# Optimization experiments

Measured on AMD Instinct MI355X. Metric: run time of the kernel, lower is better.

The kernel has to match this reference:

```python
import jax, jax.numpy as jnp
import numpy as np
from functools import partial

B, EMB, H, V, T = 128, 512, 1024, 8192, 100
START_VALUE = 0


def setup_inputs() -> dict:
    key = jax.random.key(0)
    ks = jax.random.split(key, 8)
    s = 0.05
    return {
        "x": jax.random.normal(ks[0], (B, H), jnp.float32),
        "emb_table": jax.random.normal(ks[1], (V, EMB), jnp.float32) * s,
        "w_ih": jax.random.normal(ks[2], (3 * H, EMB), jnp.float32) * s,
        "w_hh": jax.random.normal(ks[3], (3 * H, H), jnp.float32) * s,
        "b_ih": jax.random.normal(ks[4], (3 * H,), jnp.float32) * s,
        "b_hh": jax.random.normal(ks[5], (3 * H,), jnp.float32) * s,
        "cls_w": jax.random.normal(ks[6], (V, H), jnp.float32) * s,
        "cls_b": jax.random.normal(ks[7], (V,), jnp.float32) * s,
    }


def _gru_cell(e, h, w_ih, w_hh, b_ih, b_hh):
    # PyTorch GRU cell math. e: [B,EMB], h: [B,H]
    gi = e @ w_ih.T + b_ih  # [B, 3H]
    gh = h @ w_hh.T + b_hh  # [B, 3H]
    i_r, i_z, i_n = jnp.split(gi, 3, axis=1)
    h_r, h_z, h_n = jnp.split(gh, 3, axis=1)
    r = jax.nn.sigmoid(i_r + h_r)
    z = jax.nn.sigmoid(i_z + h_z)
    n = jnp.tanh(i_n + r * h_n)
    return (1.0 - z) * n + z * h


def reference(x, emb_table, w_ih, w_hh, b_ih, b_hh, cls_w, cls_b):
    # start distribution: log_softmax of one-hot at START_VALUE
    start_val = jax.nn.log_softmax(
        jnp.zeros((V,), x.dtype).at[START_VALUE].set(1.0), axis=0
    )
    prev0 = jnp.broadcast_to(start_val, (B, V))

    def step(carry, _):
        h, prev_logp = carry
        idx = jnp.argmax(prev_logp, axis=1)          # [B]
        e = emb_table[idx]                           # [B, EMB]
        h_new = _gru_cell(e, h, w_ih, w_hh, b_ih, b_hh)
        logp = jax.nn.log_softmax(h_new @ cls_w.T + cls_b, axis=1)  # [B, V]
        return (h_new, logp), logp

    _, outs = jax.lax.scan(step, (x, prev0), None, length=T - 1)
    outs = jnp.transpose(outs, (1, 0, 2))            # [B, T-1, V]
    return jnp.concatenate([prev0[:, None, :], outs], axis=1)  # [B, T, V]
```

## Files before the change

kernel.cpp:

```cpp
#include <hip/hip_runtime.h>
#include <stdint.h>


#define Bb   128
#define EMBd 512
#define Hd   1024
#define Vd   8192
#define Td   100
#define HPB  524288

typedef __attribute__((ext_vector_type(8))) _Float16 half8;
typedef __attribute__((ext_vector_type(4))) float f32x4;
typedef unsigned long long ull;

#define LOSCALE 2048.0f
#define LOINV   (1.0f/2048.0f)

#define WAITV(N) do { asm volatile("s_waitcnt vmcnt(" #N ")" ::: "memory"); \
                      __builtin_amdgcn_sched_barrier(0); } while (0)

__device__ __forceinline__ uint32_t fkey(float f) {
  uint32_t u = __float_as_uint(f);
  return (u & 0x80000000u) ? ~u : (u | 0x80000000u);
}
__device__ __forceinline__ ull umax64(ull a, ull b) { return a > b ? a : b; }

__device__ __forceinline__ void dma16(const void* g, void* l) {
  __builtin_amdgcn_global_load_lds((const uint32_t*)g, (uint32_t*)l, 16, 0, 0);
}
__device__ __forceinline__ void st16sc(void* p, half8 v) {
  f32x4 d = *(f32x4*)&v;
  asm volatile("global_store_dwordx4 %0, %1, off sc0 sc1"
               :: "v"(p), "v"(d) : "memory");
}
__device__ __forceinline__ ull sysld64(const ull* p) {
  return __hip_atomic_load((ull*)p, __ATOMIC_RELAXED, __HIP_MEMORY_SCOPE_SYSTEM);
}
__device__ __forceinline__ uint32_t ld32sys(uint32_t* p) {
  return __hip_atomic_load(p, __ATOMIC_RELAXED, __HIP_MEMORY_SCOPE_SYSTEM);
}
__device__ __forceinline__ void st32sys(uint32_t* p, uint32_t v) {
  __hip_atomic_store(p, v, __ATOMIC_RELAXED, __HIP_MEMORY_SCOPE_SYSTEM);
}
__device__ __forceinline__ uint32_t add32sys(uint32_t* p, uint32_t v) {
  return __hip_atomic_fetch_add(p, v, __ATOMIC_RELAXED, __HIP_MEMORY_SCOPE_SYSTEM);
}

__device__ __forceinline__ void cvt8(const float4 v0, const float4 v1,
                                     half8& hh, half8& ll) {
  float vv[8] = {v0.x, v0.y, v0.z, v0.w, v1.x, v1.y, v1.z, v1.w};
#pragma unroll
  for (int i = 0; i < 8; ++i) {
    _Float16 h = (_Float16)vv[i];
    hh[i] = h;
    ll[i] = (_Float16)((vv[i] - (float)h) * LOSCALE);
  }
}

__global__ void k_init(const float* __restrict__ x, float* __restrict__ hbuf0,
                       ull* __restrict__ amax, char* __restrict__ hpre0,
                       uint32_t* __restrict__ bar) {
  int tid = blockIdx.x * 256 + threadIdx.x;
  if (tid < Bb * Hd) hbuf0[tid] = x[tid];
  if (tid < Td * Bb) amax[tid] = (tid < Bb) ? 0xFFFFFFFFull : 0ull;
  if (tid >= 16384 && tid < 16640)
    bar[tid - 16384] = (tid - 16384 == 8) ? 128u : 0u;
  if (tid < 16384) {
    int b = tid & 127, sc = tid >> 7;
    int st = sc >> 2, c = sc & 3;
    const float* src = x + b * Hd + st * 32 + c * 8;
    float4 v0 = *(const float4*)src, v1 = *(const float4*)(src + 4);
    half8 hh, ll; cvt8(v0, v1, hh, ll);
    char* hp = hpre0 + st * 16384 + b * 128;
    *(half8*)(hp + ((c       ^ (b & 7))) * 16) = hh;
    *(half8*)(hp + (((c + 4) ^ (b & 7))) * 16) = ll;
  }
}

__global__ void k_prep_emb(const float* __restrict__ emb, char* __restrict__ embp) {
  int t = blockIdx.x * 256 + threadIdx.x;
  int row = t >> 6, rem = t & 63, st = rem >> 2, c = rem & 3;
  const float* src = emb + (size_t)row * EMBd + st * 32 + c * 8;
  float4 v0 = *(const float4*)src, v1 = *(const float4*)(src + 4);
  half8 hh, ll; cvt8(v0, v1, hh, ll);
  char* d = embp + (size_t)row * 2048 + st * 128;
  *(half8*)(d + c * 16) = hh;
  *(half8*)(d + (c + 4) * 16) = ll;
}

__global__ void k_prep_w(const float* __restrict__ w_ih, const float* __restrict__ w_hh,
                         char* __restrict__ wpre) {
  int bi = blockIdx.x;
  int st = bi % 12, t2 = bi / 12, q = t2 & 3, cg = t2 >> 2;
  int t = threadIdx.x; if (t >= 192) return;
  int r = t >> 2, c = t & 3;
  int g = r >> 4, bn = r & 15;
  int k0 = q * 384 + st * 32 + c * 8;
  const float* src = (k0 < 512)
    ? (w_ih + (size_t)(g * 1024 + cg * 16 + bn) * EMBd + k0)
    : (w_hh + (size_t)(g * 1024 + cg * 16 + bn) * Hd + (k0 - 512));
  float4 v0 = *(const float4*)src, v1 = *(const float4*)(src + 4);
  half8 hh, ll; cvt8(v0, v1, hh, ll);
  char* d = wpre + (size_t)bi * 6144 + r * 128;
  *(half8*)(d + ((c       ^ (r & 7))) * 16) = hh;
  *(half8*)(d + (((c + 4) ^ (r & 7))) * 16) = ll;
}

__global__ void k_prep_cls(const float* __restrict__ cls_w, char* __restrict__ clsp) {
  int b = blockIdx.x;
  int ct = b >> 5, st = b & 31;
  int t = threadIdx.x;
  int r = t >> 2, c = t & 3;
  const float* src = cls_w + (size_t)(ct * 64 + r) * Hd + st * 32 + c * 8;
  float4 v0 = *(const float4*)src, v1 = *(const float4*)(src + 4);
  half8 hh, ll; cvt8(v0, v1, hh, ll);
  char* d = clsp + (size_t)b * 8192 + r * 128;
  *(half8*)(d + ((c       ^ (r & 7))) * 16) = hh;
  *(half8*)(d + (((c + 4) ^ (r & 7))) * 16) = ll;
}

__global__ __launch_bounds__(256, 2) void k_prep_gi(
    const char* __restrict__ embp, const char* __restrict__ wpre,
    const float* __restrict__ b_ih, float* __restrict__ gi)
{
  const int cg = blockIdx.x, vh = blockIdx.y;
  const int tid = threadIdx.x, lane = tid & 63, w = tid >> 6;
  const int C = cg * 16;
  __shared__ __align__(16) char pA[4 * 8192];
  __shared__ __align__(16) char pB[4 * 6144];

  f32x4 accH[3], accL[3];
#pragma unroll
  for (int g = 0; g < 3; ++g) {
    accH[g] = (f32x4){0.f, 0.f, 0.f, 0.f};
    accL[g] = (f32x4){0.f, 0.f, 0.f, 0.f};
  }

  const int rr = lane >> 3, cc = lane & 7;
  const char* abase = embp + (size_t)(vh * 64 + w * 16 + rr) * 2048 + ((cc ^ rr) * 16);

  auto issue = [&](int st) {
    char* da = pA + (st & 3) * 8192 + w * 2048;
    const char* s0 = abase + st * 128;
    dma16(s0, da);
    dma16(s0 + 8 * 2048, da + 1024);
    const int wq = st / 12, wst = st - wq * 12;
    const char* sb = wpre + (size_t)((cg * 4 + wq) * 12 + wst) * 6144 + w * 1536 + lane * 16;
    char* db = pB + (st & 3) * 6144 + w * 1536;
    dma16(sb, db);
    if (lane < 32) dma16(sb + 1024, db + 1024);
  };

  const int l15 = lane & 15, qd = lane >> 4, r7 = l15 & 7;
  const int offAH = (w * 16 + l15) * 128 + ((qd)     ^ r7) * 16;
  const int offAL = (w * 16 + l15) * 128 + ((qd + 4) ^ r7) * 16;

  issue(0); issue(1); issue(2);
  WAITV(8);
  __builtin_amdgcn_s_barrier();

  for (int st = 0; st < 16; ++st) {
    const int bf = st & 3;
    half8 aH = *(half8*)&pA[bf * 8192 + offAH];
    half8 aL = *(half8*)&pA[bf * 8192 + offAL];
    if (st + 3 < 16) issue(st + 3);
#pragma unroll
    for (int g = 0; g < 3; ++g) {
      half8 bH = *(half8*)&pB[bf * 6144 + (g * 16 + l15) * 128 + ((qd)     ^ r7) * 16];
      half8 bL = *(half8*)&pB[bf * 6144 + (g * 16 + l15) * 128 + ((qd + 4) ^ r7) * 16];
      accH[g] = __builtin_amdgcn_mfma_f32_16x16x32_f16(aH, bH, accH[g], 0, 0, 0);
      accL[g] = __builtin_amdgcn_mfma_f32_16x16x32_f16(aH, bL, accL[g], 0, 0, 0);
      accL[g] = __builtin_amdgcn_mfma_f32_16x16x32_f16(aL, bH, accL[g], 0, 0, 0);
    }
    if (st < 15) {
      if (st <= 12)      { WAITV(8); }
      else if (st == 13) { WAITV(4); }
      else               { WAITV(0); }
      asm volatile("s_waitcnt lgkmcnt(0)" ::: "memory");
      __builtin_amdgcn_sched_barrier(0);
      __builtin_amdgcn_s_barrier();
    }
  }

  const int v0 = vh * 64 + w * 16 + qd * 4;
#pragma unroll
  for (int g = 0; g < 3; ++g) {
    float bi = b_ih[g * 1024 + C + l15];
#pragma unroll
    for (int i = 0; i < 4; ++i) {
      float val = accH[g][i] + accL[g][i] * LOINV + bi;
      gi[(size_t)(v0 + i) * 3072 + g * 1024 + C + l15] = val;
    }
  }
}

__global__ __launch_bounds__(256) void k_loop(
    const char* __restrict__ wpre, const char* __restrict__ clsp,
    const float* __restrict__ gi,
    const float* __restrict__ b_hh, const float* __restrict__ cls_b,
    float* __restrict__ hbuf, char* __restrict__ hpre,
    ull* __restrict__ amax, float* __restrict__ out,
    uint32_t* __restrict__ bar)
{
  const int wg = blockIdx.x;
  const int tid = threadIdx.x, lane = tid & 63, w = tid >> 6;
  __shared__ __align__(16) char smem[149504];

  if (tid == 0)
    (void)__hip_atomic_load(&bar[200], __ATOMIC_ACQUIRE, __HIP_MEMORY_SCOPE_AGENT);
  __syncthreads();

  uint32_t* gCnt   = &bar[0];
  uint32_t* hReady = &bar[1];
  uint32_t* aCnt   = &bar[8];

  const int l15 = lane & 15, qd = lane >> 4, r7 = l15 & 7;
  const int offA_H = (w * 16 + l15) * 128 + ((qd)     ^ r7) * 16;
  const int offA_L = (w * 16 + l15) * 128 + ((qd + 4) ^ r7) * 16;

  if (wg < 128) {
    const int cg = wg & 63, rh = wg >> 6;
    const int C = cg * 16;
    char* gA = smem;
    char* gB = smem + 49152;

    for (int s = 1; s < Td; ++s) {
      if (tid == 0)
        while (ld32sys(hReady) < (uint32_t)(s - 1)) __builtin_amdgcn_s_sleep(2);
      __syncthreads();

      const char* hsrc = hpre + (size_t)(s - 1) * HPB + rh * 8192 + w * 2048 + lane * 16;

      f32x4 accH[3], accL[3];
#pragma unroll
      for (int g = 0; g < 3; ++g) {
        accH[g] = (f32x4){0.f, 0.f, 0.f, 0.f};
        accL[g] = (f32x4){0.f, 0.f, 0.f, 0.f};
      }

      auto issue = [&](int st) {
        const int bf = st % 6;
        char* da = gA + bf * 8192 + w * 2048;
        const char* sa = hsrc + st * 16384;
        dma16(sa, da);
        dma16(sa + 1024, da + 1024);
        const int k0 = 512 + st * 32;
        const int wq = (k0 >= 1152) ? 3 : (k0 >= 768 ? 2 : 1);
        const int wst = (k0 - wq * 384) >> 5;
        const char* sb = wpre + (size_t)((cg * 4 + wq) * 12 + wst) * 6144 + w * 1536 + lane * 16;
        char* db = gB + bf * 6144 + w * 1536;
        dma16(sb, db);
        if (lane < 32) dma16(sb + 1024, db + 1024);
      };

      issue(0); issue(1); issue(2); issue(3); issue(4);

      for (int st = 0; st < 32; ++st) {
        if (st <= 27)      { WAITV(12); }
        else if (st == 28) { WAITV(9); }
        else if (st == 29) { WAITV(6); }
        else if (st == 30) { WAITV(3); }
        else               { WAITV(0); }
        __builtin_amdgcn_s_barrier();

        const int bf = st % 6;
        half8 aH = *(half8*)&gA[bf * 8192 + offA_H];
        half8 aL = *(half8*)&gA[bf * 8192 + offA_L];
        if (st + 5 < 32) issue(st + 5);
#pragma unroll
        for (int g = 0; g < 3; ++g) {
          half8 bH = *(half8*)&gB[bf * 6144 + (g * 16 + l15) * 128 + ((qd)     ^ r7) * 16];
          half8 bL = *(half8*)&gB[bf * 6144 + (g * 16 + l15) * 128 + ((qd + 4) ^ r7) * 16];
          accH[g] = __builtin_amdgcn_mfma_f32_16x16x32_f16(aH, bH, accH[g], 0, 0, 0);
          accL[g] = __builtin_amdgcn_mfma_f32_16x16x32_f16(aH, bL, accL[g], 0, 0, 0);
          accL[g] = __builtin_amdgcn_mfma_f32_16x16x32_f16(aL, bH, accL[g], 0, 0, 0);
        }
      }

      if (tid == 0)
        while (ld32sys(&aCnt[s - 1]) < 128u) __builtin_amdgcn_s_sleep(2);
      __syncthreads();

      const int j = C + l15;
      const float bh0 = b_hh[j], bh1 = b_hh[1024 + j], bh2 = b_hh[2048 + j];
      const float* hprev_f = hbuf + (size_t)((s - 1) & 1) * Bb * Hd;
      float* hnew_f = hbuf + (size_t)(s & 1) * Bb * Hd;
      const ull* amax_prev = amax + (size_t)(s - 1) * Bb;
      float outs[4];
#pragma unroll
      for (int i = 0; i < 4; ++i) {
        const int ri = rh * 64 + w * 16 + qd * 4 + i;
        const uint32_t idx = (~(uint32_t)sysld64(&amax_prev[ri])) & 8191u;
        const float* gp = gi + (size_t)idx * 3072 + j;
        float i_r = gp[0], i_z = gp[1024], i_n = gp[2048];
        float h_r = accH[0][i] + accL[0][i] * LOINV + bh0;
        float h_z = accH[1][i] + accL[1][i] * LOINV + bh1;
        float h_n = accH[2][i] + accL[2][i] * LOINV + bh2;
        float rr2 = 1.f / (1.f + expf(-(i_r + h_r)));
        float zz = 1.f / (1.f + expf(-(i_z + h_z)));
        float nn = tanhf(i_n + rr2 * h_n);
        float o = (1.f - zz) * nn + zz * hprev_f[ri * Hd + j];
        hnew_f[ri * Hd + j] = o;
        outs[i] = o;
      }
      __syncthreads();
      float* sT = (float*)smem;
#pragma unroll
      for (int i = 0; i < 4; ++i)
        sT[(w * 16 + qd * 4 + i) * 16 + l15] = outs[i];
      __syncthreads();
      if (tid < 128) {
        const int row = tid >> 1, half = tid & 1;
        const int b = rh * 64 + row;
        const float* srcp = sT + row * 16 + half * 8;
        half8 hh, ll;
#pragma unroll
        for (int e = 0; e < 8; ++e) {
          float o = srcp[e];
          _Float16 oh = (_Float16)o;
          hh[e] = oh;
          ll[e] = (_Float16)((o - (float)oh) * LOSCALE);
        }
        const int stp = C >> 5;
        const int chb = ((C & 31) >> 3) + half;
        char* hp = hpre + (size_t)s * HPB + stp * 16384 + b * 128;
        st16sc(hp + ((chb       ^ (b & 7))) * 16, hh);
        st16sc(hp + (((chb + 4) ^ (b & 7))) * 16, ll);
      }
      WAITV(0);
      __syncthreads();
      if (tid == 0) {
        uint32_t old = add32sys(gCnt, 1u);
        if (old + 1u == 128u * (uint32_t)s)
          st32sys(hReady, (uint32_t)s);
      }
    }
  } else {
    const int wgC = wg - 128;
    const int ct2 = wgC & 63, rt0 = wgC >> 6;
    const int r0c = rt0 * 64;
    char* cA = smem;
    char* cB = smem + 49152;
    const char* bb0 = clsp + (size_t)(2 * ct2)     * 262144 + w * 2048 + lane * 16;
    const char* bb1 = clsp + (size_t)(2 * ct2 + 1) * 262144 + w * 2048 + lane * 16;

    for (int s = 1; s < Td; ++s) {
      if (tid == 0)
        while (ld32sys(hReady) < (uint32_t)s) __builtin_amdgcn_s_sleep(2);
      __syncthreads();

      const char* asrc = hpre + (size_t)s * HPB + rt0 * 8192 + w * 2048 + lane * 16;

      f32x4 accH[8], accL[8];
#pragma unroll
      for (int i = 0; i < 8; ++i) {
        accH[i] = (f32x4){0.f, 0.f, 0.f, 0.f};
        accL[i] = (f32x4){0.f, 0.f, 0.f, 0.f};
      }

      auto issue = [&](int st) {
        const int bf = st % 6;
        char* da = cA + bf * 8192 + w * 2048;
        const char* sa = asrc + st * 16384;
        dma16(sa, da);
        dma16(sa + 1024, da + 1024);
        char* db = cB + bf * 16384 + w * 2048;
        const char* s0 = bb0 + st * 8192;
        dma16(s0, db);
        dma16(s0 + 1024, db + 1024);
        const char* s1 = bb1 + st * 8192;
        dma16(s1, db + 8192);
        dma16(s1 + 1024, db + 8192 + 1024);
      };

      issue(0); issue(1); issue(2); issue(3); issue(4);

      for (int st = 0; st < 32; ++st) {
        if (st <= 27)      { WAITV(24); }
        else if (st == 28) { WAITV(18); }
        else if (st == 29) { WAITV(12); }
        else if (st == 30) { WAITV(6); }
        else               { WAITV(0); }
        __builtin_amdgcn_s_barrier();

        const int bf = st % 6;
        half8 aH = *(half8*)&cA[bf * 8192 + offA_H];
        half8 aL = *(half8*)&cA[bf * 8192 + offA_L];
        if (st + 5 < 32) issue(st + 5);
#pragma unroll
        for (int cf = 0; cf < 8; ++cf) {
          const int bo = bf * 16384 + (cf >> 2) * 8192 + ((cf & 3) * 16 + l15) * 128;
          half8 bH = *(half8*)&cB[bo + ((qd)     ^ r7) * 16];
          half8 bL = *(half8*)&cB[bo + ((qd + 4) ^ r7) * 16];
          accH[cf] = __builtin_amdgcn_mfma_f32_16x16x32_f16(aH, bH, accH[cf], 0, 0, 0);
          accL[cf] = __builtin_amdgcn_mfma_f32_16x16x32_f16(aH, bL, accL[cf], 0, 0, 0);
          accL[cf] = __builtin_amdgcn_mfma_f32_16x16x32_f16(aL, bH, accL[cf], 0, 0, 0);
        }
      }

      float bsv[8];
#pragma unroll
      for (int cf = 0; cf < 8; ++cf)
        bsv[cf] = cls_b[(2 * ct2 + (cf >> 2)) * 64 + (cf & 3) * 16 + l15];
#pragma unroll
      for (int i = 0; i < 4; ++i) {
        const int brow = r0c + w * 16 + qd * 4 + i;
        float* orow = out + ((size_t)brow * Td + s) * Vd;
        ull best = 0ull;
#pragma unroll
        for (int cf = 0; cf < 8; ++cf) {
          const int v = (2 * ct2 + (cf >> 2)) * 64 + (cf & 3) * 16 + l15;
          float val = accH[cf][i] + accL[cf][i] * LOINV + bsv[cf];
          __builtin_nontemporal_store(val, &orow[v]);
          best = umax64(best, ((ull)fkey(val) << 32) | (uint32_t)(~(uint32_t)v));
        }
        best = umax64(best, __shfl_xor(best, 1));
        best = umax64(best, __shfl_xor(best, 2));
        best = umax64(best, __shfl_xor(best, 4));
        best = umax64(best, __shfl_xor(best, 8));
        if (l15 == 0) atomicMax(&amax[(size_t)s * Bb + brow], best);
      }
      WAITV(0);
      __syncthreads();
      if (tid == 0) add32sys(&aCnt[s], 1u);
    }
  }
}

__global__ void k_softmax(float* __restrict__ out,
                          const ull* __restrict__ amax) {
  int blk = blockIdx.x;
  int t = blk % Td, b = blk / Td;
  int tid = threadIdx.x;
  float* row = out + ((size_t)b * Td + t) * Vd;
  if (t == 0) {
    float lse0 = logf(expf(1.0f) + (float)(Vd - 1));
    for (int i = tid; i < Vd; i += 256) row[i] = ((i == 0) ? 1.0f : 0.0f) - lse0;
    return;
  }
  ull key = amax[t * Bb + b];
  uint32_t ku = (uint32_t)(key >> 32);
  uint32_t u = (ku & 0x80000000u) ? (ku & 0x7fffffffu) : ~ku;
  float m = __uint_as_float(u);
  float x[32];
  float ssum = 0.f;
#pragma unroll
  for (int i = 0; i < 32; ++i) {
    x[i] = row[tid + i * 256];
    ssum += expf(x[i] - m);
  }
  ssum += __shfl_xor(ssum, 1);
  ssum += __shfl_xor(ssum, 2);
  ssum += __shfl_xor(ssum, 4);
  ssum += __shfl_xor(ssum, 8);
  ssum += __shfl_xor(ssum, 16);
  ssum += __shfl_xor(ssum, 32);
  __shared__ float wsum[4];
  if ((tid & 63) == 0) wsum[tid >> 6] = ssum;
  __syncthreads();
  float lse = m + logf(wsum[0] + wsum[1] + wsum[2] + wsum[3]);
#pragma unroll
  for (int i = 0; i < 32; ++i) row[tid + i * 256] = x[i] - lse;
}

extern "C" void kernel_launch(void* const* d_in, const int* in_sizes, int n_in,
                              void* d_out, int out_size, void* d_ws, size_t ws_size,
                              hipStream_t stream) {
  const float* x     = (const float*)d_in[0];
  const float* emb   = (const float*)d_in[1];
  const float* w_ih  = (const float*)d_in[2];
  const float* w_hh  = (const float*)d_in[3];
  const float* b_ih  = (const float*)d_in[4];
  const float* b_hh  = (const float*)d_in[5];
  const float* cls_w = (const float*)d_in[6];
  const float* cls_b = (const float*)d_in[7];
  float* out = (float*)d_out;

  char* ws = (char*)d_ws;
  size_t o = 0;
  ull*      amax = (ull*)(ws + o);      o += (size_t)Td * Bb * 8;
  uint32_t* bar  = (uint32_t*)(ws + o); o += 1024;
  float*    hbuf = (float*)(ws + o);    o += (size_t)2 * Bb * Hd * 4;
  char*     hpre = ws + o;              o += (size_t)Td * HPB;
  char*     embp = ws + o;              o += (size_t)Vd * 2048;
  char*     wpre = ws + o;              o += (size_t)3072 * 6144;
  char*     clsp = ws + o;              o += (size_t)128 * 32 * 8192;
  float*    gi   = (float*)(ws + o);    o += (size_t)Vd * 3072 * 4;

  k_init<<<512, 256, 0, stream>>>(x, hbuf, amax, hpre, bar);
  k_prep_emb<<<2048, 256, 0, stream>>>(emb, embp);
  k_prep_w<<<3072, 256, 0, stream>>>(w_ih, w_hh, wpre);
  k_prep_cls<<<4096, 256, 0, stream>>>(cls_w, clsp);
  k_prep_gi<<<dim3(64, 128), 256, 0, stream>>>(embp, wpre, b_ih, gi);

  k_loop<<<256, 256, 0, stream>>>(wpre, clsp, gi, b_hh, cls_b,
                                  hbuf, hpre, amax, out, bar);

  k_softmax<<<12800, 256, 0, stream>>>(out, amax);
}
```

Before: 4.524 ms.

## Use hierarchical padded barrier counters and pad argmax slots to avoid atomic contention

Replaces the single global arrival counters for the GRU and classifier groups with a two-level tree. Groups of 8 workgroups first increment their own counter, each padded to 128 bytes, and the last arrival bumps a top-level counter. The per-row argmax atomicMax slots are also spaced 128 bytes apart so that concurrent atomics from different rows do not share a cache line. The aim is to cut serialization of contended atomics on the per-step critical path, at the cost of an extra atomic hop for the last arrival and a larger workspace.

Measured after the change: 3.849 ms. 1.18x faster.

```diff
diff --git a/kernel.cpp b/kernel.cpp
--- a/kernel.cpp
+++ b/kernel.cpp
@@ -8,6 +8,7 @@
 #define Vd   8192
 #define Td   100
 #define HPB  524288
+#define AST  16
 
 typedef __attribute__((ext_vector_type(8))) _Float16 half8;
 typedef __attribute__((ext_vector_type(4))) float f32x4;
@@ -15,6 +16,8 @@
 
 #define LOSCALE 2048.0f
 #define LOINV   (1.0f/2048.0f)
+
+#define BAR_WORDS 65536
 
 #define WAITV(N) do { asm volatile("s_waitcnt vmcnt(" #N ")" ::: "memory"); \
                       __builtin_amdgcn_sched_barrier(0); } while (0)
@@ -62,9 +65,10 @@
                        uint32_t* __restrict__ bar) {
   int tid = blockIdx.x * 256 + threadIdx.x;
   if (tid < Bb * Hd) hbuf0[tid] = x[tid];
-  if (tid < Td * Bb) amax[tid] = (tid < Bb) ? 0xFFFFFFFFull : 0ull;
-  if (tid >= 16384 && tid < 16640)
-    bar[tid - 16384] = (tid - 16384 == 8) ? 128u : 0u;
+  if (tid < Td * Bb)
+    amax[(size_t)tid * AST] = (tid < Bb) ? 0xFFFFFFFFull : 0ull;
+  if (tid < BAR_WORDS)
+    bar[tid] = (tid == 1024) ? 16u : 0u;
   if (tid < 16384) {
     int b = tid & 127, sc = tid >> 7;
     int st = sc >> 2, c = sc & 3;
@@ -207,12 +211,10 @@
   __shared__ __align__(16) char smem[149504];
 
   if (tid == 0)
-    (void)__hip_atomic_load(&bar[200], __ATOMIC_ACQUIRE, __HIP_MEMORY_SCOPE_AGENT);
+    (void)__hip_atomic_load(&bar[576], __ATOMIC_ACQUIRE, __HIP_MEMORY_SCOPE_AGENT);
   __syncthreads();
 
-  uint32_t* gCnt   = &bar[0];
-  uint32_t* hReady = &bar[1];
-  uint32_t* aCnt   = &bar[8];
+  uint32_t* hReady = &bar[544];
 
   const int l15 = lane & 15, qd = lane >> 4, r7 = l15 & 7;
   const int offA_H = (w * 16 + l15) * 128 + ((qd)     ^ r7) * 16;
@@ -278,19 +280,19 @@
       }
 
       if (tid == 0)
-        while (ld32sys(&aCnt[s - 1]) < 128u) __builtin_amdgcn_s_sleep(2);
+        while (ld32sys(&bar[1024 + (s - 1) * 32]) < 16u) __builtin_amdgcn_s_sleep(2);
       __syncthreads();
 
       const int j = C + l15;
       const float bh0 = b_hh[j], bh1 = b_hh[1024 + j], bh2 = b_hh[2048 + j];
       const float* hprev_f = hbuf + (size_t)((s - 1) & 1) * Bb * Hd;
       float* hnew_f = hbuf + (size_t)(s & 1) * Bb * Hd;
-      const ull* amax_prev = amax + (size_t)(s - 1) * Bb;
+      const ull* amax_prev = amax + (size_t)(s - 1) * Bb * AST;
       float outs[4];
 #pragma unroll
       for (int i = 0; i < 4; ++i) {
         const int ri = rh * 64 + w * 16 + qd * 4 + i;
-        const uint32_t idx = (~(uint32_t)sysld64(&amax_prev[ri])) & 8191u;
+        const uint32_t idx = (~(uint32_t)sysld64(&amax_prev[(size_t)ri * AST])) & 8191u;
         const float* gp = gi + (size_t)idx * 3072 + j;
         float i_r = gp[0], i_z = gp[1024], i_n = gp[2048];
         float h_r = accH[0][i] + accL[0][i] * LOINV + bh0;
@@ -330,9 +332,12 @@
       WAITV(0);
       __syncthreads();
       if (tid == 0) {
-        uint32_t old = add32sys(gCnt, 1u);
-        if (old + 1u == 128u * (uint32_t)s)
-          st32sys(hReady, (uint32_t)s);
+        uint32_t old = add32sys(&bar[(wg >> 3) * 32], 1u);
+        if (old + 1u == 8u * (uint32_t)s) {
+          uint32_t o2 = add32sys(&bar[512], 1u);
+          if (o2 + 1u == 16u * (uint32_t)s)
+            st32sys(hReady, (uint32_t)s);
+        }
       }
     }
   } else {
@@ -418,11 +423,16 @@
         best = umax64(best, __shfl_xor(best, 2));
         best = umax64(best, __shfl_xor(best, 4));
         best = umax64(best, __shfl_xor(best, 8));
-        if (l15 == 0) atomicMax(&amax[(size_t)s * Bb + brow], best);
+        if (l15 == 0)
+          atomicMax(&amax[((size_t)s * Bb + brow) * AST], best);
       }
       WAITV(0);
       __syncthreads();
-      if (tid == 0) add32sys(&aCnt[s], 1u);
+      if (tid == 0) {
+        uint32_t old = add32sys(&bar[8192 + ((s * 16) + (wgC >> 3)) * 32], 1u);
+        if (old + 1u == 8u)
+          add32sys(&bar[1024 + s * 32], 1u);
+      }
     }
   }
 }
@@ -438,7 +448,7 @@
     for (int i = tid; i < Vd; i += 256) row[i] = ((i == 0) ? 1.0f : 0.0f) - lse0;
     return;
   }
-  ull key = amax[t * Bb + b];
+  ull key = amax[((size_t)t * Bb + b) * AST];
   uint32_t ku = (uint32_t)(key >> 32);
   uint32_t u = (ku & 0x80000000u) ? (ku & 0x7fffffffu) : ~ku;
   float m = __uint_as_float(u);
@@ -478,8 +488,8 @@
 
   char* ws = (char*)d_ws;
   size_t o = 0;
-  ull*      amax = (ull*)(ws + o);      o += (size_t)Td * Bb * 8;
-  uint32_t* bar  = (uint32_t*)(ws + o); o += 1024;
+  ull*      amax = (ull*)(ws + o);      o += (size_t)Td * Bb * AST * 8;
+  uint32_t* bar  = (uint32_t*)(ws + o); o += (size_t)BAR_WORDS * 4;
   float*    hbuf = (float*)(ws + o);    o += (size_t)2 * Bb * Hd * 4;
   char*     hpre = ws + o;              o += (size_t)Td * HPB;
   char*     embp = ws + o;              o += (size_t)Vd * 2048;
```
